# Performance work log

Hardware: AMD Instinct MI355X
Metric: run time of the kernel (lower is better)

The kernel has to match this reference:

```python
import jax, jax.numpy as jnp
import numpy as np

N = 2048          # num_points
H = 128
W = 128
T = 2             # frames
DEG = 2           # polynomial degree (coeff rows = DEG + 1)


def setup_inputs() -> dict:
    key = jax.random.key(0)
    k1, k2, k3, k4, k5, k6 = jax.random.split(key, 6)
    # xyz: c0 = atanh(2*(rand-0.5)) as in __init__ (keep away from +-1), higher orders small
    u = jax.random.uniform(k1, (N, 2), minval=0.02, maxval=0.98)
    xyz_c0 = jnp.arctanh(2.0 * (u - 0.5))
    xyz_hi = 0.1 * jax.random.normal(k2, (DEG, N, 2))
    xyz_coeffs = jnp.concatenate([xyz_c0[None], xyz_hi], axis=0).astype(jnp.float32)
    # cholesky: c0 = [1,0,1] + 0.01*randn, higher orders small
    chol_c0 = jnp.array([1.0, 0.0, 1.0])[None, :] + 0.01 * jax.random.normal(k3, (N, 3))
    chol_hi = 0.05 * jax.random.normal(k4, (DEG, N, 3))
    cholesky_coeffs = jnp.concatenate([chol_c0[None], chol_hi], axis=0).astype(jnp.float32)
    # opacity coeffs (c0 zeros in __init__, use small noise for non-trivial grads)
    opacity_coeffs = (0.5 * jax.random.normal(k5, (DEG + 1, N, 1))).astype(jnp.float32)
    features_dc = jax.random.normal(k6, (N, 3)).astype(jnp.float32)
    t_values = jnp.linspace(0.0, 1.0, T).astype(jnp.float32)
    return {
        "xyz_coeffs": xyz_coeffs,
        "cholesky_coeffs": cholesky_coeffs,
        "opacity_coeffs": opacity_coeffs,
        "features_dc": features_dc,
        "t_values": t_values,
    }


def _forward(xyz_coeffs, cholesky_coeffs, opacity_coeffs, features_dc, t_values):
    deg_p1 = xyz_coeffs.shape[0]
    # t_power_matrix: [T, deg+1]
    tp = t_values[:, None] ** jnp.arange(deg_p1, dtype=t_values.dtype)[None, :]
    # polynomial trajectories
    xy = jnp.tanh(jnp.einsum("td,dnc->tnc", tp, xyz_coeffs))            # [T,N,2] in (-1,1)
    mx = 0.5 * (xy[..., 0] + 1.0) * W                                    # [T,N] pixel x
    my = 0.5 * (xy[..., 1] + 1.0) * H                                    # [T,N] pixel y
    chol = jnp.einsum("td,dnk->tnk", tp, cholesky_coeffs)
    chol = chol + jnp.array([0.5, 0.0, 0.5], dtype=chol.dtype)           # cholesky bound
    l0, l1, l2 = chol[..., 0], chol[..., 1], chol[..., 2]
    # Sigma = L L^T with L = [[l0,0],[l1,l2]]
    s11 = l0 * l0
    s12 = l0 * l1
    s22 = l1 * l1 + l2 * l2
    det = s11 * s22 - s12 * s12
    ca = s22 / det                                                       # conic a
    cb = -s12 / det                                                      # conic b
    cc = s11 / det                                                       # conic c
    opac = jax.nn.sigmoid(jnp.einsum("td,dnk->tnk", tp, opacity_coeffs))[..., 0]  # [T,N]
    colors = jax.nn.sigmoid(features_dc)                                 # [N,3]
    px = jnp.arange(W, dtype=mx.dtype) + 0.5                             # pixel centers
    py = jnp.arange(H, dtype=mx.dtype) + 0.5

    def render_frame(mx_t, my_t, a_t, b_t, c_t, op_t):
        dx = mx_t[:, None] - px[None, :]                                 # [N,W]
        dy = my_t[:, None] - py[None, :]                                 # [N,H]
        # quadratic form per (n,h,w): a*dx^2 + 2*b*dx*dy + c*dy^2
        q = (a_t[:, None, None] * (dx * dx)[:, None, :]
             + 2.0 * b_t[:, None, None] * dy[:, :, None] * dx[:, None, :]
             + c_t[:, None, None] * (dy * dy)[:, :, None])               # [N,H,W]
        wgt = jnp.exp(-0.5 * q) * op_t[:, None, None]                    # [N,H,W]
        return jnp.einsum("nhw,nc->chw", wgt, colors)                    # [3,H,W]

    imgs = jax.vmap(render_frame)(mx, my, ca, cb, cc, opac)              # [T,3,H,W]
    return jnp.clip(imgs, 0.0, 1.0)


def reference(xyz_coeffs, cholesky_coeffs, opacity_coeffs, features_dc, t_values):
    return _forward(xyz_coeffs, cholesky_coeffs, opacity_coeffs, features_dc, t_values)
```

## Files before the change

### kernel.cpp

```cpp
#include <hip/hip_runtime.h>

#define N_PTS  2048
#define T_FR   2
#define IMG    128
#define HW     (IMG * IMG)
#define BLOCK  512
#define WAVES  8
#define SEG    256
#define QCUT   36.043653f

#if defined(__has_builtin)
#if __has_builtin(__builtin_amdgcn_exp2f)
#define FAST_EXP2(x) __builtin_amdgcn_exp2f(x)
#endif
#endif
#ifndef FAST_EXP2
#define FAST_EXP2(x) exp2f(x)
#endif

__device__ __forceinline__ float sigmoid_fast(float x) {
    return 1.0f / (1.0f + FAST_EXP2(-1.44269504089f * x));
}
__device__ __forceinline__ float tanh_fast(float x) {
    return 1.0f - 2.0f / (FAST_EXP2(2.88539008178f * x) + 1.0f);
}

__launch_bounds__(BLOCK, 4)
__global__ void gi_fused(const float* __restrict__ xyz,
                         const float* __restrict__ chol,
                         const float* __restrict__ opa,
                         const float* __restrict__ feat,
                         const float* __restrict__ tv,
                         float* __restrict__ out) {
    __shared__ float4 sA[WAVES][SEG];
    __shared__ float4 sB[WAVES][SEG];
    __shared__ int    sCnt[WAVES];
    __shared__ float  red[BLOCK * 3];

    const int bid  = blockIdx.x;
    const int t    = bid >> 8;
    const int tile = bid & 255;
    const int h0   = (tile >> 4) << 3;
    const int w0   = (tile & 15) << 3;
    const int tid  = threadIdx.x;
    const int lane = tid & 63;
    const int wv   = tid >> 6;

    const float tt = tv[t];
    const float t2 = tt * tt;
    const float K  = -0.72134752044f;
    const float cx = (float)w0 + 4.0f;
    const float cy = (float)h0 + 4.0f;

    int cnt = 0;
#pragma unroll 4
    for (int j = 0; j < SEG / 64; ++j) {
        const int g = wv * SEG + j * 64 + lane;

        const float2 x0 = *(const float2*)&xyz[g * 2];
        const float2 x1 = *(const float2*)&xyz[N_PTS * 2 + g * 2];
        const float2 x2 = *(const float2*)&xyz[2 * N_PTS * 2 + g * 2];
        float mx = 64.0f * (tanh_fast(fmaf(t2, x2.x, fmaf(tt, x1.x, x0.x))) + 1.0f);
        float my = 64.0f * (tanh_fast(fmaf(t2, x2.y, fmaf(tt, x1.y, x0.y))) + 1.0f);

        float l0 = fmaf(t2, chol[2 * N_PTS * 3 + g * 3 + 0],
                   fmaf(tt, chol[N_PTS * 3 + g * 3 + 0], chol[g * 3 + 0])) + 0.5f;
        float l1 = fmaf(t2, chol[2 * N_PTS * 3 + g * 3 + 1],
                   fmaf(tt, chol[N_PTS * 3 + g * 3 + 1], chol[g * 3 + 1]));
        float l2 = fmaf(t2, chol[2 * N_PTS * 3 + g * 3 + 2],
                   fmaf(tt, chol[N_PTS * 3 + g * 3 + 2], chol[g * 3 + 2])) + 0.5f;

        float s11 = l0 * l0;
        float s12 = l0 * l1;
        float s22 = fmaf(l1, l1, l2 * l2);

        float ex = fmaxf(fabsf(mx - cx) - 3.5f, 0.0f);
        float ey = fmaxf(fabsf(my - cy) - 3.5f, 0.0f);
        bool hit = (ex * ex <= QCUT * s11) && (ey * ey <= QCUT * s22);

        unsigned long long m = __ballot(hit);
        if (hit) {
            float det  = fmaf(s11, s22, -s12 * s12);
            float Kinv = K / det;
            float po = fmaf(t2, opa[2 * N_PTS + g], fmaf(tt, opa[N_PTS + g], opa[g]));
            float op = sigmoid_fast(po);
            int pos = cnt + (int)__popcll(m & ((1ull << lane) - 1ull));
            sA[wv][pos] = make_float4(mx, my, s22 * Kinv, -2.0f * s12 * Kinv);
            sB[wv][pos] = make_float4(s11 * Kinv,
                                      op * sigmoid_fast(feat[g * 3 + 0]),
                                      op * sigmoid_fast(feat[g * 3 + 1]),
                                      op * sigmoid_fast(feat[g * 3 + 2]));
        }
        cnt += (int)__popcll(m);
    }
    if (lane == 0) sCnt[wv] = cnt;
    __syncthreads();

    const float px = (float)(w0 + (lane & 7)) + 0.5f;
    const float py = (float)(h0 + (lane >> 3)) + 0.5f;
    const int   L  = __builtin_amdgcn_readfirstlane(sCnt[wv]);

    float ar0 = 0.0f, ag0 = 0.0f, ab0 = 0.0f;
    float ar1 = 0.0f, ag1 = 0.0f, ab1 = 0.0f;
    int i = 0;
    for (; i + 1 < L; i += 2) {
        float4 A0 = sA[wv][i],     B0 = sB[wv][i];
        float4 A1 = sA[wv][i + 1], B1 = sB[wv][i + 1];
        float dx0 = A0.x - px, dy0 = A0.y - py;
        float dx1 = A1.x - px, dy1 = A1.y - py;
        float q0 = fmaf(B0.x * dy0, dy0, fmaf(A0.w, dy0, A0.z * dx0) * dx0);
        float q1 = fmaf(B1.x * dy1, dy1, fmaf(A1.w, dy1, A1.z * dx1) * dx1);
        float w0g = FAST_EXP2(q0);
        float w1g = FAST_EXP2(q1);
        ar0 = fmaf(w0g, B0.y, ar0); ag0 = fmaf(w0g, B0.z, ag0); ab0 = fmaf(w0g, B0.w, ab0);
        ar1 = fmaf(w1g, B1.y, ar1); ag1 = fmaf(w1g, B1.z, ag1); ab1 = fmaf(w1g, B1.w, ab1);
    }
    if (i < L) {
        float4 A0 = sA[wv][i], B0 = sB[wv][i];
        float dx0 = A0.x - px, dy0 = A0.y - py;
        float q0 = fmaf(B0.x * dy0, dy0, fmaf(A0.w, dy0, A0.z * dx0) * dx0);
        float w0g = FAST_EXP2(q0);
        ar0 = fmaf(w0g, B0.y, ar0); ag0 = fmaf(w0g, B0.z, ag0); ab0 = fmaf(w0g, B0.w, ab0);
    }

    red[tid * 3 + 0] = ar0 + ar1;
    red[tid * 3 + 1] = ag0 + ag1;
    red[tid * 3 + 2] = ab0 + ab1;
    __syncthreads();

    if (tid < 192) {
        const int ch = tid >> 6;
        const int p  = tid & 63;
        float acc = 0.0f;
#pragma unroll
        for (int w8 = 0; w8 < WAVES; ++w8)
            acc += red[(w8 * 64 + p) * 3 + ch];
        const int h   = h0 + (p >> 3);
        const int w   = w0 + (p & 7);
        out[(t * 3 + ch) * HW + h * IMG + w] = fminf(fmaxf(acc, 0.0f), 1.0f);
    }
}

extern "C" void kernel_launch(void* const* d_in, const int* in_sizes, int n_in,
                              void* d_out, int out_size, void* d_ws, size_t ws_size,
                              hipStream_t stream) {
    const float* xyz  = (const float*)d_in[0];
    const float* chol = (const float*)d_in[1];
    const float* opa  = (const float*)d_in[2];
    const float* feat = (const float*)d_in[3];
    const float* tv   = (const float*)d_in[4];

    gi_fused<<<T_FR * 256, BLOCK, 0, stream>>>(
        xyz, chol, opa, feat, tv, (float*)d_out);
}
```

Baseline: 13.36 us.

## Enlarge pixel tile to 16x8 with two pixels per lane

Each block now covers a 16x8 pixel tile instead of 8x8, and each lane computes two pixels (rows y and y+4) from the same gaussian load, sharing the dx terms. The grid is halved, which roughly halves the per-tile culling work of re-evaluating all 2048 gaussians per block. In exchange the culling box is looser, so more gaussians pass per tile and some evaluated weights fall outside their footprint. The grid drops to 256 blocks and register pressure rises; launch bounds are relaxed to match.

Result: faster. 11.79 us (-11.8%).

```diff
diff --git a/kernel.cpp b/kernel.cpp
--- a/kernel.cpp
+++ b/kernel.cpp
@@ -25,7 +25,7 @@
     return 1.0f - 2.0f / (FAST_EXP2(2.88539008178f * x) + 1.0f);
 }
 
-__launch_bounds__(BLOCK, 4)
+__launch_bounds__(BLOCK, 2)
 __global__ void gi_fused(const float* __restrict__ xyz,
                          const float* __restrict__ chol,
                          const float* __restrict__ opa,
@@ -35,13 +35,13 @@
     __shared__ float4 sA[WAVES][SEG];
     __shared__ float4 sB[WAVES][SEG];
     __shared__ int    sCnt[WAVES];
-    __shared__ float  red[BLOCK * 3];
+    __shared__ float  red[WAVES][128][3];
 
     const int bid  = blockIdx.x;
-    const int t    = bid >> 8;
-    const int tile = bid & 255;
-    const int h0   = (tile >> 4) << 3;
-    const int w0   = (tile & 15) << 3;
+    const int t    = bid >> 7;
+    const int tile = bid & 127;
+    const int w0   = (tile & 7) << 4;
+    const int h0   = (tile >> 3) << 3;
     const int tid  = threadIdx.x;
     const int lane = tid & 63;
     const int wv   = tid >> 6;
@@ -49,7 +49,7 @@
     const float tt = tv[t];
     const float t2 = tt * tt;
     const float K  = -0.72134752044f;
-    const float cx = (float)w0 + 4.0f;
+    const float cx = (float)w0 + 8.0f;
     const float cy = (float)h0 + 4.0f;
 
     int cnt = 0;
@@ -74,7 +74,7 @@
         float s12 = l0 * l1;
         float s22 = fmaf(l1, l1, l2 * l2);
 
-        float ex = fmaxf(fabsf(mx - cx) - 3.5f, 0.0f);
+        float ex = fmaxf(fabsf(mx - cx) - 7.5f, 0.0f);
         float ey = fmaxf(fabsf(my - cy) - 3.5f, 0.0f);
         bool hit = (ex * ex <= QCUT * s11) && (ey * ey <= QCUT * s22);
 
@@ -96,47 +96,62 @@
     if (lane == 0) sCnt[wv] = cnt;
     __syncthreads();
 
-    const float px = (float)(w0 + (lane & 7)) + 0.5f;
-    const float py = (float)(h0 + (lane >> 3)) + 0.5f;
-    const int   L  = __builtin_amdgcn_readfirstlane(sCnt[wv]);
+    const float px  = (float)(w0 + (lane & 15)) + 0.5f;
+    const float py0 = (float)(h0 + (lane >> 4)) + 0.5f;
+    const float py1 = py0 + 4.0f;
+    const int   L   = __builtin_amdgcn_readfirstlane(sCnt[wv]);
 
-    float ar0 = 0.0f, ag0 = 0.0f, ab0 = 0.0f;
-    float ar1 = 0.0f, ag1 = 0.0f, ab1 = 0.0f;
+    float r00 = 0, g00 = 0, b00 = 0, r01 = 0, g01 = 0, b01 = 0;
+    float r10 = 0, g10 = 0, b10 = 0, r11 = 0, g11 = 0, b11 = 0;
     int i = 0;
     for (; i + 1 < L; i += 2) {
         float4 A0 = sA[wv][i],     B0 = sB[wv][i];
         float4 A1 = sA[wv][i + 1], B1 = sB[wv][i + 1];
-        float dx0 = A0.x - px, dy0 = A0.y - py;
-        float dx1 = A1.x - px, dy1 = A1.y - py;
-        float q0 = fmaf(B0.x * dy0, dy0, fmaf(A0.w, dy0, A0.z * dx0) * dx0);
-        float q1 = fmaf(B1.x * dy1, dy1, fmaf(A1.w, dy1, A1.z * dx1) * dx1);
-        float w0g = FAST_EXP2(q0);
-        float w1g = FAST_EXP2(q1);
-        ar0 = fmaf(w0g, B0.y, ar0); ag0 = fmaf(w0g, B0.z, ag0); ab0 = fmaf(w0g, B0.w, ab0);
-        ar1 = fmaf(w1g, B1.y, ar1); ag1 = fmaf(w1g, B1.z, ag1); ab1 = fmaf(w1g, B1.w, ab1);
+
+        float dx0 = A0.x - px, az0 = A0.z * dx0;
+        float dA0 = A0.y - py0, dB0 = A0.y - py1;
+        float qA0 = fmaf(B0.x * dA0, dA0, fmaf(A0.w, dA0, az0) * dx0);
+        float qB0 = fmaf(B0.x * dB0, dB0, fmaf(A0.w, dB0, az0) * dx0);
+        float wA0 = FAST_EXP2(qA0), wB0 = FAST_EXP2(qB0);
+        r00 = fmaf(wA0, B0.y, r00); g00 = fmaf(wA0, B0.z, g00); b00 = fmaf(wA0, B0.w, b00);
+        r01 = fmaf(wB0, B0.y, r01); g01 = fmaf(wB0, B0.z, g01); b01 = fmaf(wB0, B0.w, b01);
+
+        float dx1 = A1.x - px, az1 = A1.z * dx1;
+        float dA1 = A1.y - py0, dB1 = A1.y - py1;
+        float qA1 = fmaf(B1.x * dA1, dA1, fmaf(A1.w, dA1, az1) * dx1);
+        float qB1 = fmaf(B1.x * dB1, dB1, fmaf(A1.w, dB1, az1) * dx1);
+        float wA1 = FAST_EXP2(qA1), wB1 = FAST_EXP2(qB1);
+        r10 = fmaf(wA1, B1.y, r10); g10 = fmaf(wA1, B1.z, g10); b10 = fmaf(wA1, B1.w, b10);
+        r11 = fmaf(wB1, B1.y, r11); g11 = fmaf(wB1, B1.z, g11); b11 = fmaf(wB1, B1.w, b11);
     }
     if (i < L) {
         float4 A0 = sA[wv][i], B0 = sB[wv][i];
-        float dx0 = A0.x - px, dy0 = A0.y - py;
-        float q0 = fmaf(B0.x * dy0, dy0, fmaf(A0.w, dy0, A0.z * dx0) * dx0);
-        float w0g = FAST_EXP2(q0);
-        ar0 = fmaf(w0g, B0.y, ar0); ag0 = fmaf(w0g, B0.z, ag0); ab0 = fmaf(w0g, B0.w, ab0);
+        float dx0 = A0.x - px, az0 = A0.z * dx0;
+        float dA0 = A0.y - py0, dB0 = A0.y - py1;
+        float qA0 = fmaf(B0.x * dA0, dA0, fmaf(A0.w, dA0, az0) * dx0);
+        float qB0 = fmaf(B0.x * dB0, dB0, fmaf(A0.w, dB0, az0) * dx0);
+        float wA0 = FAST_EXP2(qA0), wB0 = FAST_EXP2(qB0);
+        r00 = fmaf(wA0, B0.y, r00); g00 = fmaf(wA0, B0.z, g00); b00 = fmaf(wA0, B0.w, b00);
+        r01 = fmaf(wB0, B0.y, r01); g01 = fmaf(wB0, B0.z, g01); b01 = fmaf(wB0, B0.w, b01);
     }
 
-    red[tid * 3 + 0] = ar0 + ar1;
-    red[tid * 3 + 1] = ag0 + ag1;
-    red[tid * 3 + 2] = ab0 + ab1;
+    red[wv][lane][0]      = r00 + r10;
+    red[wv][lane][1]      = g00 + g10;
+    red[wv][lane][2]      = b00 + b10;
+    red[wv][lane + 64][0] = r01 + r11;
+    red[wv][lane + 64][1] = g01 + g11;
+    red[wv][lane + 64][2] = b01 + b11;
     __syncthreads();
 
-    if (tid < 192) {
-        const int ch = tid >> 6;
-        const int p  = tid & 63;
+    if (tid < 384) {
+        const int ch = tid >> 7;
+        const int p  = tid & 127;
         float acc = 0.0f;
 #pragma unroll
         for (int w8 = 0; w8 < WAVES; ++w8)
-            acc += red[(w8 * 64 + p) * 3 + ch];
-        const int h   = h0 + (p >> 3);
-        const int w   = w0 + (p & 7);
+            acc += red[w8][p][ch];
+        const int h = h0 + (p >> 4);
+        const int w = w0 + (p & 15);
         out[(t * 3 + ch) * HW + h * IMG + w] = fminf(fmaxf(acc, 0.0f), 1.0f);
     }
 }
@@ -150,6 +165,6 @@
     const float* feat = (const float*)d_in[3];
     const float* tv   = (const float*)d_in[4];
 
-    gi_fused<<<T_FR * 256, BLOCK, 0, stream>>>(
+    gi_fused<<<T_FR * 128, BLOCK, 0, stream>>>(
         xyz, chol, opa, feat, tv, (float*)d_out);
 }
```
